# Optimization experiments

Measured on AMD Instinct MI355X. Metric: run time of the kernel, lower is better.

Reference implementation:

```python
import jax, jax.numpy as jnp
import numpy as np

# Instant-NGP / tcnn hash grid encoding constants (from init_kwargs)
L = 16           # n_levels
F = 2            # n_features_per_level
T = 2 ** 15      # hashmap size per level
DIM = 3
BASE = 16.0      # base_resolution
FINEST = 512.0   # finest_resolution
RANGE = 1.0
B = (FINEST / BASE) ** (1.0 / (L - 1))  # per_level_scale
N_POINTS = 500000
# tcnn spatial hash primes (first dim uses 1)
PRIMES = jnp.array([1, 2654435761, 805459861], dtype=jnp.uint32)


def setup_inputs() -> dict:
    key = jax.random.key(0)
    k1, k2 = jax.random.split(key)
    x = jax.random.uniform(k1, (N_POINTS, DIM), dtype=jnp.float32)  # points in [0,1)
    table = jax.random.normal(k2, (L, T, F), dtype=jnp.float32) * 1e-4  # tcnn-style tiny init
    return {"x": x, "table": table}


def reference(x, table):
    # wrapper: map from [-range, range] to [0, 1]
    xn = (x + RANGE) / (2.0 * RANGE)                       # [N, 3]
    n = xn.shape[0]
    # per-level grid scale (tcnn: scale = base * b^l - 1)
    scales = BASE * (B ** jnp.arange(L, dtype=jnp.float32)) - 1.0  # [L]
    pos = xn[:, None, :] * scales[None, :, None] + 0.5     # [N, L, 3]
    pos_floor = jnp.floor(pos)
    frac = pos - pos_floor                                  # [N, L, 3]
    grid = pos_floor.astype(jnp.uint32)                    # [N, L, 3]
    # 8 cube corners as binary offsets
    corners = jnp.array([[(c >> d) & 1 for d in range(DIM)] for c in range(2 ** DIM)],
                        dtype=jnp.uint32)                   # [8, 3]
    coords = grid[:, :, None, :] + corners[None, None, :, :]  # [N, L, 8, 3] uint32
    h = coords * PRIMES                                     # uint32 wraps (modular mult)
    idx = (h[..., 0] ^ h[..., 1] ^ h[..., 2]) & jnp.uint32(T - 1)  # [N, L, 8]
    # gather per-level features: [N, L, 8, F]
    feats = table[jnp.arange(L)[None, :, None], idx]
    # trilinear interpolation weights
    cf = corners.astype(jnp.float32)                        # [8, 3]
    w = jnp.prod(jnp.where(cf[None, None, :, :] == 1.0,
                           frac[:, :, None, :],
                           1.0 - frac[:, :, None, :]), axis=-1)  # [N, L, 8]
    out = jnp.einsum('nlc,nlcf->nlf', w, feats)             # [N, L, F]
    return out.reshape(n, L * F)
```

## Files before the change

kernel.cpp:

```cpp
#include <hip/hip_runtime.h>
#include <stdint.h>


constexpr int      kL  = 16;
constexpr int      kT  = 32768;
constexpr uint32_t kM  = kT - 1;
constexpr uint32_t kP1 = 2654435761u;
constexpr uint32_t kP2 = 805459861u;
constexpr int      kNC = 32;
constexpr int      kBT = 1024;

typedef float f32x4 __attribute__((ext_vector_type(4)));

__device__ __constant__ float c_scales[kL] = {
    15.0f,
    19.158736798317972f,
    24.398416831491190f,
    31.0f,
    39.317473596635944f,
    49.796833662982380f,
    63.0f,
    79.634947193271890f,
    100.59366732596477f,
    127.0f,
    160.26989438654378f,
    202.18733465192953f,
    255.0f,
    321.53978877308750f,
    405.37466930385903f,
    511.0f
};

__global__ __launch_bounds__(kBT) void level_absmax(
    const float4* __restrict__ table4,
    float*        __restrict__ scales)
{
    __shared__ float sred[16];
    int l   = blockIdx.x;
    int tid = (int)threadIdx.x;

    const float4* src = table4 + (size_t)l * (kT / 2);
    float vmax = 0.0f;
    for (int e = tid; e < kT / 2; e += kBT) {
        float4 q = src[e];
        vmax = fmaxf(vmax, fmaxf(fmaxf(fabsf(q.x), fabsf(q.y)),
                                 fmaxf(fabsf(q.z), fabsf(q.w))));
    }
#pragma unroll
    for (int off = 32; off >= 1; off >>= 1)
        vmax = fmaxf(vmax, __shfl_xor(vmax, off, 64));
    if ((tid & 63) == 0) sred[tid >> 6] = vmax;
    __syncthreads();
    if (tid < 64) {
        float v = (tid < 16) ? sred[tid] : 0.0f;
#pragma unroll
        for (int off = 8; off >= 1; off >>= 1)
            v = fmaxf(v, __shfl_xor(v, off, 64));
        if (tid == 0) scales[l] = v;
    }
}

__device__ __forceinline__ void gather_level_u8(
    const uint16_t* __restrict__ ltab,
    float A, float C, float x0, float x1, float x2,
    float& ax, float& ay)
{
    float p0 = fmaf(x0, A, C);
    float p1 = fmaf(x1, A, C);
    float p2 = fmaf(x2, A, C);

    float fl0 = floorf(p0), fl1 = floorf(p1), fl2 = floorf(p2);
    float fr0 = p0 - fl0,   fr1 = p1 - fl1,   fr2 = p2 - fl2;

    uint32_t g0 = (uint32_t)(int)fl0;
    uint32_t g1 = (uint32_t)(int)fl1;
    uint32_t g2 = (uint32_t)(int)fl2;

    uint32_t g0p = g0 + 1u;
    uint32_t hy0 = g1 * kP1;  uint32_t hy1 = hy0 + kP1;
    uint32_t hz0 = g2 * kP2;  uint32_t hz1 = hz0 + kP2;

    uint32_t hyz0 = hy0 ^ hz0;
    uint32_t hyz1 = hy1 ^ hz0;
    uint32_t hyz2 = hy0 ^ hz1;
    uint32_t hyz3 = hy1 ^ hz1;

    uint32_t ee[8];
    ee[0] = ltab[(g0  ^ hyz0) & kM];
    ee[1] = ltab[(g0p ^ hyz0) & kM];
    ee[2] = ltab[(g0  ^ hyz1) & kM];
    ee[3] = ltab[(g0p ^ hyz1) & kM];
    ee[4] = ltab[(g0  ^ hyz2) & kM];
    ee[5] = ltab[(g0p ^ hyz2) & kM];
    ee[6] = ltab[(g0  ^ hyz3) & kM];
    ee[7] = ltab[(g0p ^ hyz3) & kM];

    float wx0 = 1.0f - fr0;
    float wy0 = 1.0f - fr1;
    float wz0 = 1.0f - fr2;
    float wyz0 = wy0 * wz0;
    float wyz1 = fr1 * wz0;
    float wyz2 = wy0 * fr2;
    float wyz3 = fr1 * fr2;
    const float wf[8] = {wx0 * wyz0, fr0 * wyz0,
                         wx0 * wyz1, fr0 * wyz1,
                         wx0 * wyz2, fr0 * wyz2,
                         wx0 * wyz3, fr0 * wyz3};

    float accx = 0.0f, accy = 0.0f;
#pragma unroll
    for (int cc = 0; cc < 8; ++cc) {
        uint32_t u = ee[cc];
        accx = fmaf(wf[cc], (float)(u & 0xFFu),        accx);
        accy = fmaf(wf[cc], (float)((u >> 8) & 0xFFu), accy);
    }
    ax = accx - 127.0f;
    ay = accy - 127.0f;
}

__global__ __launch_bounds__(kBT, 4) void hashgrid_pair(
    const float*  __restrict__ x,
    const float2* __restrict__ table,
    const float*  __restrict__ lscale,
    float*        __restrict__ out,
    int n_points, int chunk_sz)
{
    __shared__ uint16_t ltab0[kT];
    __shared__ uint16_t ltab1[kT];

    int bid = blockIdx.x;
    int p   = bid >> 5;
    int c   = bid & 31;

    int tid  = (int)threadIdx.x;
    int base = c * chunk_sz;
    int lim  = min(base + chunk_sz, n_points);

    int l0 = 2 * p;
    int l1 = 2 * p + 1;

    float am0 = lscale[l0];
    float am1 = lscale[l1];
    float dq0 = am0 * (1.0f / 127.0f);
    float dq1 = am1 * (1.0f / 127.0f);
    float iv0 = am0 > 0.0f ? 127.0f / am0 : 0.0f;
    float iv1 = am1 > 0.0f ? 127.0f / am1 : 0.0f;

    {
        const float4* t0 = reinterpret_cast<const float4*>(table + (size_t)l0 * kT);
        const float4* t1 = reinterpret_cast<const float4*>(table + (size_t)l1 * kT);
        uint32_t* d0 = reinterpret_cast<uint32_t*>(ltab0);
        uint32_t* d1 = reinterpret_cast<uint32_t*>(ltab1);
        for (int e = tid; e < kT / 2; e += kBT) {
            float4 q0 = t0[e];
            float4 q1 = t1[e];
            int a0 = (int)rintf(q0.x * iv0) + 127, b0 = (int)rintf(q0.y * iv0) + 127;
            int c0 = (int)rintf(q0.z * iv0) + 127, e0 = (int)rintf(q0.w * iv0) + 127;
            int a1 = (int)rintf(q1.x * iv1) + 127, b1 = (int)rintf(q1.y * iv1) + 127;
            int c1 = (int)rintf(q1.z * iv1) + 127, e1 = (int)rintf(q1.w * iv1) + 127;
            d0[e] = ((uint32_t)a0)       | ((uint32_t)b0 << 8)
                  | ((uint32_t)c0 << 16) | ((uint32_t)e0 << 24);
            d1[e] = ((uint32_t)a1)       | ((uint32_t)b1 << 8)
                  | ((uint32_t)c1 << 16) | ((uint32_t)e1 << 24);
        }
    }
    __syncthreads();

    float s0 = c_scales[l0];
    float A0 = s0 * 0.5f;
    float C0 = fmaf(s0, 0.5f, 0.5f);
    float s1 = c_scales[l1];
    float A1 = s1 * 0.5f;
    float C1 = fmaf(s1, 0.5f, 0.5f);

    for (int n = base + tid; n < lim; n += kBT) {
        float x0 = x[n * 3 + 0];
        float x1 = x[n * 3 + 1];
        float x2 = x[n * 3 + 2];

        float a0x, a0y, a1x, a1y;
        gather_level_u8(ltab0, A0, C0, x0, x1, x2, a0x, a0y);
        gather_level_u8(ltab1, A1, C1, x0, x1, x2, a1x, a1y);

        f32x4 v;
        v.x = a0x * dq0;
        v.y = a0y * dq0;
        v.z = a1x * dq1;
        v.w = a1y * dq1;
        *reinterpret_cast<f32x4*>(out + (size_t)n * 32 + p * 4) = v;
    }
}

extern "C" void kernel_launch(void* const* d_in, const int* in_sizes, int n_in,
                              void* d_out, int out_size, void* d_ws, size_t ws_size,
                              hipStream_t stream) {
    const float*  x     = (const float*)d_in[0];
    const float2* table = (const float2*)d_in[1];
    float*        out   = (float*)d_out;
    float*        lsc   = (float*)d_ws;

    int n_points = in_sizes[0] / 3;
    int chunk_sz = (n_points + kNC - 1) / kNC;
    int blocks   = (kL / 2) * kNC;

    level_absmax<<<kL, kBT, 0, stream>>>(
        reinterpret_cast<const float4*>(table), lsc);
    hashgrid_pair<<<blocks, kBT, 0, stream>>>(
        x, table, lsc, out, n_points, chunk_sz);
}
```

Measured before the change: 40.77 us.

## Use fp16 packed nested lerp interpolation and parallelize absmax with atomics

Replaces the 8-weight trilinear sum with nested lerps. The x-axis lerp is done in packed fp16, built by splicing the u8 bytes into 0x6400-biased halves via a perm. The 127 bias and the dequant are folded into a single fma. The absmax pre-pass now runs as 256 small blocks that combine with atomicMax on the float bits, which needs an extra zeroing kernel. The aim is fewer ALU ops per gather and more parallelism in the pre-pass, at the cost of an extra launch and fp16 rounding of the x-interpolation.

```diff
diff --git a/kernel.cpp b/kernel.cpp
--- a/kernel.cpp
+++ b/kernel.cpp
@@ -1,4 +1,5 @@
 #include <hip/hip_runtime.h>
+#include <hip/hip_fp16.h>
 #include <stdint.h>
 
 
@@ -31,39 +32,40 @@
     511.0f
 };
 
-__global__ __launch_bounds__(kBT) void level_absmax(
+__global__ void zero_scales(uint32_t* s) {
+    if (threadIdx.x < kL) s[threadIdx.x] = 0u;
+}
+
+__global__ __launch_bounds__(256) void level_absmax(
     const float4* __restrict__ table4,
-    float*        __restrict__ scales)
+    uint32_t*     __restrict__ scales)
 {
-    __shared__ float sred[16];
-    int l   = blockIdx.x;
+    int b  = blockIdx.x;
+    int l  = b >> 4;
+    int st = b & 15;
     int tid = (int)threadIdx.x;
 
-    const float4* src = table4 + (size_t)l * (kT / 2);
-    float vmax = 0.0f;
-    for (int e = tid; e < kT / 2; e += kBT) {
-        float4 q = src[e];
-        vmax = fmaxf(vmax, fmaxf(fmaxf(fabsf(q.x), fabsf(q.y)),
-                                 fmaxf(fabsf(q.z), fabsf(q.w))));
+    const float4* src = table4 + (size_t)l * (kT / 2) + (size_t)st * 1024;
+    float m = 0.0f;
+#pragma unroll
+    for (int i = 0; i < 4; ++i) {
+        float4 q = src[tid + 256 * i];
+        m = fmaxf(m, fmaxf(fmaxf(fabsf(q.x), fabsf(q.y)),
+                           fmaxf(fabsf(q.z), fabsf(q.w))));
     }
 #pragma unroll
     for (int off = 32; off >= 1; off >>= 1)
-        vmax = fmaxf(vmax, __shfl_xor(vmax, off, 64));
-    if ((tid & 63) == 0) sred[tid >> 6] = vmax;
-    __syncthreads();
-    if (tid < 64) {
-        float v = (tid < 16) ? sred[tid] : 0.0f;
-#pragma unroll
-        for (int off = 8; off >= 1; off >>= 1)
-            v = fmaxf(v, __shfl_xor(v, off, 64));
-        if (tid == 0) scales[l] = v;
-    }
-}
-
-__device__ __forceinline__ void gather_level_u8(
-    const uint16_t* __restrict__ ltab,
+        m = fmaxf(m, __shfl_xor(m, off, 64));
+    if ((tid & 63) == 0)
+        atomicMax(&scales[l], __float_as_uint(m));
+}
+
+__device__ __forceinline__ void gather_level(
+    const char* __restrict__ lds,
+    uint32_t slice_bit,
     float A, float C, float x0, float x1, float x2,
-    float& ax, float& ay)
+    float dq, float ob,
+    float& ox, float& oy)
 {
     float p0 = fmaf(x0, A, C);
     float p1 = fmaf(x1, A, C);
@@ -76,57 +78,54 @@
     uint32_t g1 = (uint32_t)(int)fl1;
     uint32_t g2 = (uint32_t)(int)fl2;
 
-    uint32_t g0p = g0 + 1u;
     uint32_t hy0 = g1 * kP1;  uint32_t hy1 = hy0 + kP1;
     uint32_t hz0 = g2 * kP2;  uint32_t hz1 = hz0 + kP2;
 
-    uint32_t hyz0 = hy0 ^ hz0;
-    uint32_t hyz1 = hy1 ^ hz0;
-    uint32_t hyz2 = hy0 ^ hz1;
-    uint32_t hyz3 = hy1 ^ hz1;
-
-    uint32_t ee[8];
-    ee[0] = ltab[(g0  ^ hyz0) & kM];
-    ee[1] = ltab[(g0p ^ hyz0) & kM];
-    ee[2] = ltab[(g0  ^ hyz1) & kM];
-    ee[3] = ltab[(g0p ^ hyz1) & kM];
-    ee[4] = ltab[(g0  ^ hyz2) & kM];
-    ee[5] = ltab[(g0p ^ hyz2) & kM];
-    ee[6] = ltab[(g0  ^ hyz3) & kM];
-    ee[7] = ltab[(g0p ^ hyz3) & kM];
-
-    float wx0 = 1.0f - fr0;
-    float wy0 = 1.0f - fr1;
-    float wz0 = 1.0f - fr2;
-    float wyz0 = wy0 * wz0;
-    float wyz1 = fr1 * wz0;
-    float wyz2 = wy0 * fr2;
-    float wyz3 = fr1 * fr2;
-    const float wf[8] = {wx0 * wyz0, fr0 * wyz0,
-                         wx0 * wyz1, fr0 * wyz1,
-                         wx0 * wyz2, fr0 * wyz2,
-                         wx0 * wyz3, fr0 * wyz3};
-
-    float accx = 0.0f, accy = 0.0f;
+    uint32_t gs  = ((g0 << 1) & 0xFFFEu) | slice_bit;
+    uint32_t gps = (((g0 + 1u) << 1) & 0xFFFEu) | slice_bit;
+    uint32_t hs0 = (((hy0 ^ hz0) << 1) & 0xFFFEu);
+    uint32_t hs1 = (((hy1 ^ hz0) << 1) & 0xFFFEu);
+    uint32_t hs2 = (((hy0 ^ hz1) << 1) & 0xFFFEu);
+    uint32_t hs3 = (((hy1 ^ hz1) << 1) & 0xFFFEu);
+
+    __half2 fr0h = __float2half2_rn(fr0);
+
+    float fx[4], fy[4];
+    const uint32_t hs[4] = {hs0, hs1, hs2, hs3};
 #pragma unroll
-    for (int cc = 0; cc < 8; ++cc) {
-        uint32_t u = ee[cc];
-        accx = fmaf(wf[cc], (float)(u & 0xFFu),        accx);
-        accy = fmaf(wf[cc], (float)((u >> 8) & 0xFFu), accy);
-    }
-    ax = accx - 127.0f;
-    ay = accy - 127.0f;
+    for (int j = 0; j < 4; ++j) {
+        uint32_t e0 = *(const uint16_t*)(lds + (gs  ^ hs[j]));
+        uint32_t e1 = *(const uint16_t*)(lds + (gps ^ hs[j]));
+        uint32_t u0 = __builtin_amdgcn_perm(e0, e0, 0x03010200u) | 0x64006400u;
+        uint32_t u1 = __builtin_amdgcn_perm(e1, e1, 0x03010200u) | 0x64006400u;
+        __half2 H0 = *reinterpret_cast<__half2*>(&u0);
+        __half2 H1 = *reinterpret_cast<__half2*>(&u1);
+        __half2 D  = __hsub2(H1, H0);
+        __half2 FX = __hfma2(fr0h, D, H0);
+        fx[j] = __low2float(FX);
+        fy[j] = __high2float(FX);
+    }
+
+    float fy0x = fmaf(fr1, fx[1] - fx[0], fx[0]);
+    float fy0y = fmaf(fr1, fy[1] - fy[0], fy[0]);
+    float fy1x = fmaf(fr1, fx[3] - fx[2], fx[2]);
+    float fy1y = fmaf(fr1, fy[3] - fy[2], fy[2]);
+
+    float tx = fmaf(fr2, fy1x - fy0x, fy0x);
+    float ty = fmaf(fr2, fy1y - fy0y, fy0y);
+
+    ox = fmaf(tx, dq, ob);
+    oy = fmaf(ty, dq, ob);
 }
 
 __global__ __launch_bounds__(kBT, 4) void hashgrid_pair(
-    const float*  __restrict__ x,
-    const float2* __restrict__ table,
-    const float*  __restrict__ lscale,
-    float*        __restrict__ out,
+    const float*    __restrict__ x,
+    const float2*   __restrict__ table,
+    const uint32_t* __restrict__ lscale,
+    float*          __restrict__ out,
     int n_points, int chunk_sz)
 {
-    __shared__ uint16_t ltab0[kT];
-    __shared__ uint16_t ltab1[kT];
+    __shared__ uint16_t ltab[2][kT];
 
     int bid = blockIdx.x;
     int p   = bid >> 5;
@@ -139,18 +138,20 @@
     int l0 = 2 * p;
     int l1 = 2 * p + 1;
 
-    float am0 = lscale[l0];
-    float am1 = lscale[l1];
+    float am0 = __uint_as_float(lscale[l0]);
+    float am1 = __uint_as_float(lscale[l1]);
     float dq0 = am0 * (1.0f / 127.0f);
     float dq1 = am1 * (1.0f / 127.0f);
+    float ob0 = dq0 * -1151.0f;
+    float ob1 = dq1 * -1151.0f;
     float iv0 = am0 > 0.0f ? 127.0f / am0 : 0.0f;
     float iv1 = am1 > 0.0f ? 127.0f / am1 : 0.0f;
 
     {
         const float4* t0 = reinterpret_cast<const float4*>(table + (size_t)l0 * kT);
         const float4* t1 = reinterpret_cast<const float4*>(table + (size_t)l1 * kT);
-        uint32_t* d0 = reinterpret_cast<uint32_t*>(ltab0);
-        uint32_t* d1 = reinterpret_cast<uint32_t*>(ltab1);
+        uint32_t* d0 = reinterpret_cast<uint32_t*>(&ltab[0][0]);
+        uint32_t* d1 = reinterpret_cast<uint32_t*>(&ltab[1][0]);
         for (int e = tid; e < kT / 2; e += kBT) {
             float4 q0 = t0[e];
             float4 q1 = t1[e];
@@ -166,6 +167,8 @@
     }
     __syncthreads();
 
+    const char* lds = reinterpret_cast<const char*>(&ltab[0][0]);
+
     float s0 = c_scales[l0];
     float A0 = s0 * 0.5f;
     float C0 = fmaf(s0, 0.5f, 0.5f);
@@ -179,14 +182,14 @@
         float x2 = x[n * 3 + 2];
 
         float a0x, a0y, a1x, a1y;
-        gather_level_u8(ltab0, A0, C0, x0, x1, x2, a0x, a0y);
-        gather_level_u8(ltab1, A1, C1, x0, x1, x2, a1x, a1y);
+        gather_level(lds, 0u,       A0, C0, x0, x1, x2, dq0, ob0, a0x, a0y);
+        gather_level(lds, 0x10000u, A1, C1, x0, x1, x2, dq1, ob1, a1x, a1y);
 
         f32x4 v;
-        v.x = a0x * dq0;
-        v.y = a0y * dq0;
-        v.z = a1x * dq1;
-        v.w = a1y * dq1;
+        v.x = a0x;
+        v.y = a0y;
+        v.z = a1x;
+        v.w = a1y;
         *reinterpret_cast<f32x4*>(out + (size_t)n * 32 + p * 4) = v;
     }
 }
@@ -197,13 +200,14 @@
     const float*  x     = (const float*)d_in[0];
     const float2* table = (const float2*)d_in[1];
     float*        out   = (float*)d_out;
-    float*        lsc   = (float*)d_ws;
+    uint32_t*     lsc   = (uint32_t*)d_ws;
 
     int n_points = in_sizes[0] / 3;
     int chunk_sz = (n_points + kNC - 1) / kNC;
     int blocks   = (kL / 2) * kNC;
 
-    level_absmax<<<kL, kBT, 0, stream>>>(
+    zero_scales<<<1, 64, 0, stream>>>(lsc);
+    level_absmax<<<256, 256, 0, stream>>>(
         reinterpret_cast<const float4*>(table), lsc);
     hashgrid_pair<<<blocks, kBT, 0, stream>>>(
         x, table, lsc, out, n_points, chunk_sz);
```

New measurement: 52.76 us. 1.29x slower.
